# Optimization experiments

Hardware: AMD Instinct MI355X
Metric: run time of the kernel (lower is better)

## Reference

```python
import jax, jax.numpy as jnp
import numpy as np

B, N, K, H = 8, 2048, 30, 128
SCALE = 30.0
EPS = 1e-5


def _gelu(x):
    return jax.nn.gelu(x, approximate=False)


def _lin(x, w, b):
    return x @ w.T + b


def _ln(x, g, b):
    m = x.mean(-1, keepdims=True)
    v = ((x - m) ** 2).mean(-1, keepdims=True)
    return g * (x - m) * jax.lax.rsqrt(v + EPS) + b


def _gather_nodes(h_V, E_idx):
    # h_V: [B,N,H], E_idx: [B,N,K] -> [B,N,K,H]
    b_idx = jnp.arange(h_V.shape[0])[:, None, None]
    return h_V[b_idx, E_idx]


def setup_inputs() -> dict:
    key = jax.random.key(0)
    ks = jax.random.split(key, 16)
    p = 0.02
    inp = {
        'h_V': jax.random.normal(ks[0], (B, N, H), jnp.float32),
        'h_E': jax.random.normal(ks[1], (B, N, K, H), jnp.float32),
        'E_idx': jax.random.randint(ks[2], (B, N, K), 0, N, jnp.int32),
        'mask_V': jnp.ones((B, N), jnp.float32),
        'mask_attend': jnp.ones((B, N, K), jnp.float32),
        # node message MLP (3H -> H -> H -> H)
        'W1_w': jax.random.normal(ks[3], (H, 3 * H), jnp.float32) * p,
        'W1_b': jnp.zeros((H,), jnp.float32),
        'W2_w': jax.random.normal(ks[4], (H, H), jnp.float32) * p,
        'W2_b': jnp.zeros((H,), jnp.float32),
        'W3_w': jax.random.normal(ks[5], (H, H), jnp.float32) * p,
        'W3_b': jnp.zeros((H,), jnp.float32),
        # edge message MLP (3H -> H -> H -> H)
        'W11_w': jax.random.normal(ks[6], (H, 3 * H), jnp.float32) * p,
        'W11_b': jnp.zeros((H,), jnp.float32),
        'W12_w': jax.random.normal(ks[7], (H, H), jnp.float32) * p,
        'W12_b': jnp.zeros((H,), jnp.float32),
        'W13_w': jax.random.normal(ks[8], (H, H), jnp.float32) * p,
        'W13_b': jnp.zeros((H,), jnp.float32),
        # layer norms
        'n1_g': jnp.ones((H,), jnp.float32), 'n1_b': jnp.zeros((H,), jnp.float32),
        'n2_g': jnp.ones((H,), jnp.float32), 'n2_b': jnp.zeros((H,), jnp.float32),
        'n3_g': jnp.ones((H,), jnp.float32), 'n3_b': jnp.zeros((H,), jnp.float32),
        # position-wise FFN (H -> 4H -> H)
        'din_w': jax.random.normal(ks[9], (4 * H, H), jnp.float32) * p,
        'din_b': jnp.zeros((4 * H,), jnp.float32),
        'dout_w': jax.random.normal(ks[10], (H, 4 * H), jnp.float32) * p,
        'dout_b': jnp.zeros((H,), jnp.float32),
    }
    return inp


def reference(h_V, h_E, E_idx, mask_V, mask_attend,
              W1_w, W1_b, W2_w, W2_b, W3_w, W3_b,
              W11_w, W11_b, W12_w, W12_b, W13_w, W13_b,
              n1_g, n1_b, n2_g, n2_b, n3_g, n3_b,
              din_w, din_b, dout_w, dout_b):
    k = h_E.shape[-2]
    # --- node update ---
    h_nbr = _gather_nodes(h_V, E_idx)                       # [B,N,K,H]
    h_V_exp = jnp.broadcast_to(h_V[:, :, None, :], h_nbr.shape)
    h_EV = jnp.concatenate([h_V_exp, h_nbr, h_E], axis=-1)  # [B,N,K,3H]
    h_message = _lin(_gelu(_lin(_gelu(_lin(h_EV, W1_w, W1_b)), W2_w, W2_b)), W3_w, W3_b)
    h_message = mask_attend[..., None] * h_message
    dh = jnp.sum(h_message, axis=-2) / SCALE
    h_V = _ln(h_V + dh, n1_g, n1_b)
    dh = _lin(_gelu(_lin(h_V, din_w, din_b)), dout_w, dout_b)
    h_V = _ln(h_V + dh, n2_g, n2_b)
    h_V = mask_V[..., None] * h_V
    # --- edge update ---
    h_nbr = _gather_nodes(h_V, E_idx)
    h_V_exp = jnp.broadcast_to(h_V[:, :, None, :], h_nbr.shape)
    h_EV = jnp.concatenate([h_V_exp, h_nbr, h_E], axis=-1)
    h_message = _lin(_gelu(_lin(_gelu(_lin(h_EV, W11_w, W11_b)), W12_w, W12_b)), W13_w, W13_b)
    h_E = _ln(h_E + h_message, n3_g, n3_b)
    return (h_V, h_E)
```

## Files before the change

kernel.cpp:

```cpp
#include <hip/hip_runtime.h>

#define B_ 8
#define N_ 2048
#define K_ 30
#define H_ 128
#define LDA 136
#define LDM 132
#define EPS_ 1e-5f

typedef __attribute__((ext_vector_type(8))) short short8;
typedef __attribute__((ext_vector_type(4))) float f32x4;

__device__ inline unsigned short f2bf(float f) {
  union { float f; unsigned u; } v; v.f = f;
  unsigned r = v.u + 0x7fffu + ((v.u >> 16) & 1u);
  return (unsigned short)(r >> 16);
}

__device__ inline float bf2f(unsigned short h) {
  union { unsigned u; float f; } v; v.u = ((unsigned)h) << 16; return v.f;
}

__device__ inline unsigned pkbf(float lo, float hi) {
  unsigned r;
  asm("v_cvt_pk_bf16_f32 %0, %1, %2" : "=v"(r) : "v"(lo), "v"(hi));
  return r;
}

__device__ inline float gelu_t(float x) {
  const float p = x * x;
  const float z = x * (1.5957691216057308f + 0.07135481627f * p);
  const float e = exp2f(z * -1.4426950408889634f);
  return x * __builtin_amdgcn_rcpf(1.0f + e);
}

__device__ inline short8 pack8(float4 a, float4 b) {
  short8 o;
  o[0] = (short)f2bf(a.x); o[1] = (short)f2bf(a.y); o[2] = (short)f2bf(a.z); o[3] = (short)f2bf(a.w);
  o[4] = (short)f2bf(b.x); o[5] = (short)f2bf(b.y); o[6] = (short)f2bf(b.z); o[7] = (short)f2bf(b.w);
  return o;
}

template<int LDW>
__device__ inline void gemmT(const unsigned short* __restrict__ sA,
                             const unsigned short* __restrict__ W,
                             int lane, int cb, f32x4 (&acc)[4][2]) {
  const int rl = lane & 15;
  const int klo = (lane >> 4) << 3;
#pragma unroll
  for (int ks = 0; ks < 4; ++ks) {
    short8 wf[2];
#pragma unroll
    for (int fn = 0; fn < 2; ++fn)
      wf[fn] = *(const short8*)(W + (size_t)(cb + fn * 16 + rl) * LDW + ks * 32 + klo);
#pragma unroll
    for (int et = 0; et < 4; ++et) {
      const short8 ef = *(const short8*)(sA + (et * 16 + rl) * LDA + ks * 32 + klo);
      acc[et][0] = __builtin_amdgcn_mfma_f32_16x16x32_bf16(wf[0], ef, acc[et][0], 0, 0, 0);
      acc[et][1] = __builtin_amdgcn_mfma_f32_16x16x32_bf16(wf[1], ef, acc[et][1], 0, 0, 0);
    }
  }
}

#define ZERO42(A) \
  _Pragma("unroll") for (int e_ = 0; e_ < 4; ++e_) { A[e_][0] = (f32x4){0,0,0,0}; A[e_][1] = (f32x4){0,0,0,0}; }

template<int LDW, int NN>
__device__ inline void gemm64(const unsigned short* __restrict__ sA,
                              const unsigned short* __restrict__ W,
                              int lane, int cb, f32x4 (&acc)[4][NN]) {
  const int rl = lane & 15;
  const int klo = (lane >> 4) << 3;
#pragma unroll
  for (int ks = 0; ks < 4; ++ks) {
    short8 a[4];
#pragma unroll
    for (int m = 0; m < 4; ++m)
      a[m] = *(const short8*)(sA + (m * 16 + rl) * LDA + ks * 32 + klo);
#pragma unroll
    for (int n = 0; n < NN; ++n) {
      const short8 b8 = *(const short8*)(W + (size_t)(cb + n * 16 + rl) * LDW + ks * 32 + klo);
#pragma unroll
      for (int m = 0; m < 4; ++m)
        acc[m][n] = __builtin_amdgcn_mfma_f32_16x16x32_bf16(a[m], b8, acc[m][n], 0, 0, 0);
    }
  }
}

__global__ __launch_bounds__(256) void prep(const float* __restrict__ w1, const float* __restrict__ w2,
                                            const float* __restrict__ w3, const float* __restrict__ w11,
                                            const float* __restrict__ w12, const float* __restrict__ w13,
                                            const float* __restrict__ din, const float* __restrict__ dout,
                                            unsigned short* __restrict__ dst) {
  const int i = blockIdx.x * 256 + threadIdx.x;
  const float* s; int off;
  if (i < 49152)       { s = w1;  off = 0; }
  else if (i < 65536)  { s = w2;  off = 49152; }
  else if (i < 81920)  { s = w3;  off = 65536; }
  else if (i < 131072) { s = w11; off = 81920; }
  else if (i < 147456) { s = w12; off = 131072; }
  else if (i < 163840) { s = w13; off = 147456; }
  else if (i < 229376) { s = din; off = 163840; }
  else                 { s = dout; off = 229376; }
  dst[i] = f2bf(s[i - off]);
}

template<bool F32SRC, bool SPLIT>
__global__ __launch_bounds__(256) void preY(const void* __restrict__ Xv,
                                            const unsigned short* __restrict__ Wbase,
                                            unsigned short* __restrict__ Yc,
                                            unsigned short* __restrict__ Yn) {
  __shared__ __align__(16) unsigned short sA[64 * LDA];
  const int tid = threadIdx.x;
  const int lane = tid & 63;
  const int w = tid >> 6;
  const int rows = blockIdx.x << 6;
  const int rl = lane & 15;
  const int h4 = (lane >> 4) << 2;

  if (F32SRC) {
    const float* X = (const float*)Xv;
    for (int t = tid; t < 1024; t += 256) {
      const int r = t >> 4, seg = t & 15;
      const float* src = X + (((size_t)(rows + r)) << 7) + seg * 8;
      *(short8*)(sA + r * LDA + seg * 8) = pack8(*(const float4*)src, *(const float4*)(src + 4));
    }
  } else {
    const unsigned short* X = (const unsigned short*)Xv;
    for (int t = tid; t < 1024; t += 256) {
      const int r = t >> 4, seg = t & 15;
      *(short8*)(sA + r * LDA + seg * 8) =
          *(const short8*)(X + (((size_t)(rows + r)) << 7) + seg * 8);
    }
  }
  __syncthreads();

  const int half = w >> 1;
  const int cb = (w & 1) * 64;
  f32x4 acc[4][4];
#pragma unroll
  for (int m = 0; m < 4; ++m)
#pragma unroll
    for (int n = 0; n < 4; ++n) acc[m][n] = (f32x4){0, 0, 0, 0};
  gemm64<384, 4>(sA, Wbase + half * 128, lane, cb, acc);

  unsigned short* Y = half ? Yn : Yc;
  const int stride = SPLIT ? 128 : 256;
  const int coff = SPLIT ? 0 : half * 128;
#pragma unroll
  for (int n = 0; n < 4; ++n) {
    const int col = coff + cb + n * 16 + rl;
#pragma unroll
    for (int m = 0; m < 4; ++m)
#pragma unroll
      for (int i = 0; i < 4; ++i)
        Y[(size_t)(rows + m * 16 + h4 + i) * stride + col] = f2bf(acc[m][n][i]);
  }
}

__global__ __launch_bounds__(256, 4) void k1(
    const float* __restrict__ hV, const float* __restrict__ hE,
    const int* __restrict__ Eidx, const float* __restrict__ mattend,
    const unsigned short* __restrict__ wc, const unsigned short* __restrict__ Y1,
    const float* __restrict__ W1b, const float* __restrict__ W2b,
    const float* __restrict__ W3b, const float* __restrict__ n1g,
    const float* __restrict__ n1b, unsigned short* __restrict__ hV1b,
    float* __restrict__ outE) {
  __shared__ __align__(16) unsigned short sBuf[2 * 64 * LDA];
  __shared__ __align__(16) unsigned short sYc[2 * 128];
  __shared__ float sMask[64];
  __shared__ float sRed[2][128];
  unsigned short* sE = sBuf;
  unsigned short* sG = sBuf + 64 * LDA;
  float* sM = (float*)sBuf;

  const int tid = threadIdx.x;
  const int lane = tid & 63;
  const int w = tid >> 6;
  const int rl = lane & 15;
  const int h4 = (lane >> 4) << 2;
  const int bid = (blockIdx.x & 7) * 1024 + (blockIdx.x >> 3);
  const int v0 = bid << 1;
  const int b = v0 >> 11;
  const int n0 = v0 & (N_ - 1);
  const int bBase = b * N_;

  const unsigned short* W1c = wc;
  const unsigned short* W2c = wc + 49152;
  const unsigned short* W3c = wc + 65536;

  for (int t = tid; t < 1024; t += 256) {
    const int r = t >> 4, seg = t & 15;
    const int g = r >> 5, kk = r & 31;
    const int kc = kk < K_ ? kk : K_ - 1;
    const size_t e = (size_t)(bBase + n0 + g) * K_ + kc;
    const float* src = hE + (e << 7) + seg * 8;
    const short8 o = pack8(*(const float4*)src, *(const float4*)(src + 4));
    *(short8*)(sE + r * LDA + seg * 8) = o;
    if (kk < K_)
      *(short8*)((unsigned short*)(outE + (e << 7)) + 128 + seg * 8) = o;
  }
  for (int t = tid; t < 1024; t += 256) {
    const int r = t >> 4, seg = t & 15;
    const int g = r >> 5;
    int kk = r & 31; if (kk >= K_) kk = K_ - 1;
    const int j = Eidx[(bBase + n0 + g) * K_ + kk];
    *(short8*)(sG + r * LDA + seg * 8) =
        *(const short8*)(Y1 + (size_t)(bBase + j) * 256 + 128 + seg * 8);
  }
  {
    const int g = tid >> 7, c = tid & 127;
    sYc[g * 128 + c] = Y1[(size_t)(bBase + n0 + g) * 256 + c];
  }
  if (tid < 64) {
    const int g = tid >> 5, kk = tid & 31;
    sMask[tid] = (kk < K_) ? mattend[(bBase + n0 + g) * K_ + kk] : 0.f;
  }
  __syncthreads();

  f32x4 acc[4][2];
  ZERO42(acc)
  gemmT<384>(sE, W1c + 256, lane, w * 32, acc);

  {
    float4 b1v[2];
    b1v[0] = *(const float4*)(W1b + w * 32 + h4);
    b1v[1] = *(const float4*)(W1b + w * 32 + 16 + h4);
#pragma unroll
    for (int et = 0; et < 4; ++et) {
      const int e = et * 16 + rl;
      const int g = et >> 1;
#pragma unroll
      for (int fn = 0; fn < 2; ++fn) {
        const int f0 = w * 32 + fn * 16 + h4;
        const ushort4 yc = *(const ushort4*)(sYc + g * 128 + f0);
        const ushort4 yn = *(const ushort4*)(sG + e * LDA + f0);
        const float x0 = gelu_t(acc[et][fn][0] + b1v[fn].x + bf2f(yc.x) + bf2f(yn.x));
        const float x1 = gelu_t(acc[et][fn][1] + b1v[fn].y + bf2f(yc.y) + bf2f(yn.y));
        const float x2 = gelu_t(acc[et][fn][2] + b1v[fn].z + bf2f(yc.z) + bf2f(yn.z));
        const float x3 = gelu_t(acc[et][fn][3] + b1v[fn].w + bf2f(yc.w) + bf2f(yn.w));
        uint2 o; o.x = pkbf(x0, x1); o.y = pkbf(x2, x3);
        *(uint2*)(sG + e * LDA + f0) = o;
      }
    }
  }
  __syncthreads();

  f32x4 acc2[4][2];
  ZERO42(acc2)
  gemmT<128>(sG, W2c, lane, w * 32, acc2);
  __syncthreads();
  {
    float4 b2v[2];
    b2v[0] = *(const float4*)(W2b + w * 32 + h4);
    b2v[1] = *(const float4*)(W2b + w * 32 + 16 + h4);
#pragma unroll
    for (int et = 0; et < 4; ++et) {
      const int e = et * 16 + rl;
#pragma unroll
      for (int fn = 0; fn < 2; ++fn) {
        const int f0 = w * 32 + fn * 16 + h4;
        const float x0 = gelu_t(acc2[et][fn][0] + b2v[fn].x);
        const float x1 = gelu_t(acc2[et][fn][1] + b2v[fn].y);
        const float x2 = gelu_t(acc2[et][fn][2] + b2v[fn].z);
        const float x3 = gelu_t(acc2[et][fn][3] + b2v[fn].w);
        uint2 o; o.x = pkbf(x0, x1); o.y = pkbf(x2, x3);
        *(uint2*)(sG + e * LDA + f0) = o;
      }
    }
  }
  __syncthreads();

  f32x4 acc3[4][2];
  ZERO42(acc3)
  gemmT<128>(sG, W3c, lane, w * 32, acc3);
  __syncthreads();

  {
    float4 b3v[2];
    b3v[0] = *(const float4*)(W3b + w * 32 + h4);
    b3v[1] = *(const float4*)(W3b + w * 32 + 16 + h4);
#pragma unroll
    for (int et = 0; et < 4; ++et) {
      const int e = et * 16 + rl;
      const float mk = sMask[e];
#pragma unroll
      for (int fn = 0; fn < 2; ++fn) {
        const int f0 = w * 32 + fn * 16 + h4;
        const float4 v = make_float4((acc3[et][fn][0] + b3v[fn].x) * mk,
                                     (acc3[et][fn][1] + b3v[fn].y) * mk,
                                     (acc3[et][fn][2] + b3v[fn].z) * mk,
                                     (acc3[et][fn][3] + b3v[fn].w) * mk);
        *(float4*)(sM + e * LDM + f0) = v;
      }
    }
  }
  __syncthreads();

  {
    const int g = tid >> 7, f = tid & 127;
    float s = 0.f;
#pragma unroll
    for (int kk = 0; kk < 32; ++kk) s += sM[(g * 32 + kk) * LDM + f];
    sRed[g][f] = s;
  }
  __syncthreads();

  if (w < 2) {
    const size_t base = ((size_t)(bBase + n0 + w)) << 7;
    const float x0 = hV[base + lane] + sRed[w][lane] * (1.0f / 30.0f);
    const float x1 = hV[base + 64 + lane] + sRed[w][64 + lane] * (1.0f / 30.0f);
    float s = x0 + x1;
#pragma unroll
    for (int o = 1; o < 64; o <<= 1) s += __shfl_xor(s, o);
    const float mean = s * (1.0f / 128.0f);
    const float d0 = x0 - mean, d1 = x1 - mean;
    float vs = d0 * d0 + d1 * d1;
#pragma unroll
    for (int o = 1; o < 64; o <<= 1) vs += __shfl_xor(vs, o);
    const float inv = rsqrtf(vs * (1.0f / 128.0f) + EPS_);
    hV1b[base + lane] = f2bf(n1g[lane] * (d0 * inv) + n1b[lane]);
    hV1b[base + 64 + lane] = f2bf(n1g[64 + lane] * (d1 * inv) + n1b[64 + lane]);
  }
}

__global__ __launch_bounds__(256) void k2(
    const unsigned short* __restrict__ hV1b, const unsigned short* __restrict__ wc,
    const float* __restrict__ dinb, const float* __restrict__ doutb,
    const float* __restrict__ n2g, const float* __restrict__ n2b,
    const float* __restrict__ maskV, float* __restrict__ outV,
    unsigned short* __restrict__ hV2c) {
  __shared__ __align__(16) unsigned short sT[16 * LDA];
  __shared__ float sStat[16][2][4];

  const int tid = threadIdx.x;
  const int lane = tid & 63;
  const int w = tid >> 6;
  const int rl = lane & 15;
  const int h4 = (lane >> 4) << 2;
  const int klo = (lane >> 4) << 3;
  const int rowbase = blockIdx.x << 4;

  const unsigned short* dinc = wc + 163840;
  const unsigned short* doutc = wc + 229376;

  short8 ef[4];
#pragma unroll
  for (int ks = 0; ks < 4; ++ks)
    ef[ks] = *(const short8*)(hV1b + (((size_t)(rowbase + rl)) << 7) + ks * 32 + klo);

  f32x4 acc2[2];
  acc2[0] = (f32x4){0, 0, 0, 0}; acc2[1] = (f32x4){0, 0, 0, 0};

  for (int c = 0; c < 4; ++c) {
    f32x4 acc1[2];
    acc1[0] = (f32x4){0, 0, 0, 0}; acc1[1] = (f32x4){0, 0, 0, 0};
#pragma unroll
    for (int ks = 0; ks < 4; ++ks)
#pragma unroll
      for (int fn = 0; fn < 2; ++fn) {
        const short8 wf = *(const short8*)(dinc + (size_t)(c * 128 + w * 32 + fn * 16 + rl) * 128 + ks * 32 + klo);
        acc1[fn] = __builtin_amdgcn_mfma_f32_16x16x32_bf16(wf, ef[ks], acc1[fn], 0, 0, 0);
      }
    __syncthreads();
    {
      float4 db[2];
      db[0] = *(const float4*)(dinb + c * 128 + w * 32 + h4);
      db[1] = *(const float4*)(dinb + c * 128 + w * 32 + 16 + h4);
#pragma unroll
      for (int fn = 0; fn < 2; ++fn) {
        const int f0 = w * 32 + fn * 16 + h4;
        const float x0 = gelu_t(acc1[fn][0] + db[fn].x);
        const float x1 = gelu_t(acc1[fn][1] + db[fn].y);
        const float x2 = gelu_t(acc1[fn][2] + db[fn].z);
        const float x3 = gelu_t(acc1[fn][3] + db[fn].w);
        uint2 o; o.x = pkbf(x0, x1); o.y = pkbf(x2, x3);
        *(uint2*)(sT + rl * LDA + f0) = o;
      }
    }
    __syncthreads();
#pragma unroll
    for (int ks = 0; ks < 4; ++ks) {
      const short8 xf = *(const short8*)(sT + rl * LDA + ks * 32 + klo);
#pragma unroll
      for (int fn = 0; fn < 2; ++fn) {
        const short8 wf2 = *(const short8*)(doutc + (size_t)(w * 32 + fn * 16 + rl) * 512 + c * 128 + ks * 32 + klo);
        acc2[fn] = __builtin_amdgcn_mfma_f32_16x16x32_bf16(wf2, xf, acc2[fn], 0, 0, 0);
      }
    }
  }

  const int row = rl;
  const int grow = rowbase + row;
  {
    float4 wbv[2];
    wbv[0] = *(const float4*)(doutb + w * 32 + h4);
    wbv[1] = *(const float4*)(doutb + w * 32 + 16 + h4);
    float s = 0.f, ss = 0.f;
#pragma unroll
    for (int fn = 0; fn < 2; ++fn) {
      const int f0 = w * 32 + fn * 16 + h4;
      const ushort4 rr = *(const ushort4*)(hV1b + (((size_t)grow) << 7) + f0);
      const float x0 = acc2[fn][0] + wbv[fn].x + bf2f(rr.x);
      const float x1 = acc2[fn][1] + wbv[fn].y + bf2f(rr.y);
      const float x2 = acc2[fn][2] + wbv[fn].z + bf2f(rr.z);
      const float x3 = acc2[fn][3] + wbv[fn].w + bf2f(rr.w);
      acc2[fn] = (f32x4){x0, x1, x2, x3};
      s += x0 + x1 + x2 + x3;
      ss += x0 * x0 + x1 * x1 + x2 * x2 + x3 * x3;
    }
    s += __shfl_xor(s, 16); s += __shfl_xor(s, 32);
    ss += __shfl_xor(ss, 16); ss += __shfl_xor(ss, 32);
    if (lane < 16) { sStat[row][0][w] = s; sStat[row][1][w] = ss; }
  }
  __syncthreads();
  {
    const float sum = sStat[row][0][0] + sStat[row][0][1] + sStat[row][0][2] + sStat[row][0][3];
    const float ssq = sStat[row][1][0] + sStat[row][1][1] + sStat[row][1][2] + sStat[row][1][3];
    const float mean = sum * (1.0f / 128.0f);
    const float inv = rsqrtf(ssq * (1.0f / 128.0f) - mean * mean + EPS_);
    const float mv = maskV[grow];
#pragma unroll
    for (int fn = 0; fn < 2; ++fn) {
      const int f0 = w * 32 + fn * 16 + h4;
      const float4 gv = *(const float4*)(n2g + f0);
      const float4 bv = *(const float4*)(n2b + f0);
      const float y0 = (gv.x * (acc2[fn][0] - mean) * inv + bv.x) * mv;
      const float y1 = (gv.y * (acc2[fn][1] - mean) * inv + bv.y) * mv;
      const float y2 = (gv.z * (acc2[fn][2] - mean) * inv + bv.z) * mv;
      const float y3 = (gv.w * (acc2[fn][3] - mean) * inv + bv.w) * mv;
      *(float4*)(outV + (((size_t)grow) << 7) + f0) = make_float4(y0, y1, y2, y3);
      uint2 o; o.x = pkbf(y0, y1); o.y = pkbf(y2, y3);
      *(uint2*)(hV2c + (((size_t)grow) << 7) + f0) = o;
    }
  }
}

__global__ __launch_bounds__(256, 4) void k3(
    const int* __restrict__ Eidx, const unsigned short* __restrict__ wc,
    const unsigned short* __restrict__ Y2c, const unsigned short* __restrict__ Y2n,
    const float* __restrict__ W11b, const float* __restrict__ W12b,
    const float* __restrict__ W13b, const float* __restrict__ n3g,
    const float* __restrict__ n3b, float* __restrict__ outE) {
  __shared__ __align__(16) unsigned short sE[64 * LDA];
  __shared__ __align__(16) unsigned short sG[64 * LDA];
  __shared__ unsigned short sYc[2 * 128];
  __shared__ float sStat[64][2][4];

  const int tid = threadIdx.x;
  const int lane = tid & 63;
  const int w = tid >> 6;
  const int rl = lane & 15;
  const int h4 = (lane >> 4) << 2;
  const int bid = (blockIdx.x & 7) * 1024 + (blockIdx.x >> 3);
  const int v0 = bid << 1;
  const int b = v0 >> 11;
  const int n0 = v0 & (N_ - 1);
  const int bBase = b * N_;

  const unsigned short* W11c = wc + 81920;
  const unsigned short* W12c = wc + 131072;
  const unsigned short* W13c = wc + 147456;

  for (int t = tid; t < 1024; t += 256) {
    const int r = t >> 4, seg = t & 15;
    const int g = r >> 5;
    int kk = r & 31; if (kk >= K_) kk = K_ - 1;
    const size_t e = (size_t)(bBase + n0 + g) * K_ + kk;
    *(short8*)(sE + r * LDA + seg * 8) =
        *(const short8*)((const unsigned short*)(outE + (e << 7)) + 128 + seg * 8);
  }
  for (int t = tid; t < 1024; t += 256) {
    const int r = t >> 4, seg = t & 15;
    const int g = r >> 5;
    int kk = r & 31; if (kk >= K_) kk = K_ - 1;
    const int j = Eidx[(bBase + n0 + g) * K_ + kk];
    *(short8*)(sG + r * LDA + seg * 8) =
        *(const short8*)(Y2n + (size_t)(bBase + j) * 128 + seg * 8);
  }
  {
    const int g = tid >> 7, c = tid & 127;
    sYc[g * 128 + c] = Y2c[(size_t)(bBase + n0 + g) * 128 + c];
  }
  __syncthreads();

  f32x4 acc[4][2];
  ZERO42(acc)
  gemm64<384, 2>(sE, W11c + 256, lane, w * 32, acc);

#pragma unroll
  for (int n = 0; n < 2; ++n) {
    const int f = w * 32 + n * 16 + rl;
    const float bb = W11b[f];
#pragma unroll
    for (int m = 0; m < 4; ++m)
#pragma unroll
      for (int i = 0; i < 4; ++i) {
        const int e = m * 16 + h4 + i;
        const float x = acc[m][n][i] + bb + bf2f(sYc[(e >> 5) * 128 + f]) + bf2f(sG[e * LDA + f]);
        sG[e * LDA + f] = f2bf(gelu_t(x));
      }
  }
  __syncthreads();

  f32x4 acc2[4][2];
  ZERO42(acc2)
  gemm64<128, 2>(sG, W12c, lane, w * 32, acc2);
  __syncthreads();
#pragma unroll
  for (int n = 0; n < 2; ++n) {
    const int f = w * 32 + n * 16 + rl;
    const float bb = W12b[f];
#pragma unroll
    for (int m = 0; m < 4; ++m)
#pragma unroll
      for (int i = 0; i < 4; ++i) {
        const int e = m * 16 + h4 + i;
        sG[e * LDA + f] = f2bf(gelu_t(acc2[m][n][i] + bb));
      }
  }
  __syncthreads();

  f32x4 acc3[4][2];
  ZERO42(acc3)
  gemm64<128, 2>(sG, W13c, lane, w * 32, acc3);

  float gc[2], bc[2], wb[2];
#pragma unroll
  for (int n = 0; n < 2; ++n) {
    const int f = w * 32 + n * 16 + rl;
    gc[n] = n3g[f]; bc[n] = n3b[f]; wb[n] = W13b[f];
  }
#pragma unroll
  for (int m = 0; m < 4; ++m)
#pragma unroll
    for (int i = 0; i < 4; ++i) {
      const int e = m * 16 + h4 + i;
      float s = 0.f, ss = 0.f;
#pragma unroll
      for (int n = 0; n < 2; ++n) {
        const int f = w * 32 + n * 16 + rl;
        const float x = acc3[m][n][i] + wb[n] + bf2f(sE[e * LDA + f]);
        acc3[m][n][i] = x;
        s += x; ss += x * x;
      }
#pragma unroll
      for (int o = 1; o <= 8; o <<= 1) { s += __shfl_xor(s, o); ss += __shfl_xor(ss, o); }
      if (rl == 0) { sStat[e][0][w] = s; sStat[e][1][w] = ss; }
    }
  __syncthreads();
#pragma unroll
  for (int m = 0; m < 4; ++m)
#pragma unroll
    for (int i = 0; i < 4; ++i) {
      const int e = m * 16 + h4 + i;
      const int g = e >> 5, kk = e & 31;
      if (kk >= K_) continue;
      const float sum = sStat[e][0][0] + sStat[e][0][1] + sStat[e][0][2] + sStat[e][0][3];
      const float ssq = sStat[e][1][0] + sStat[e][1][1] + sStat[e][1][2] + sStat[e][1][3];
      const float mean = sum * (1.0f / 128.0f);
      const float inv = rsqrtf(ssq * (1.0f / 128.0f) - mean * mean + EPS_);
      float* dst = outE + (((size_t)((bBase + n0 + g) * K_ + kk)) << 7) + w * 32 + rl;
#pragma unroll
      for (int n = 0; n < 2; ++n)
        dst[n * 16] = gc[n] * (acc3[m][n][i] - mean) * inv + bc[n];
    }
}

extern "C" void kernel_launch(void* const* d_in, const int* in_sizes, int n_in,
                              void* d_out, int out_size, void* d_ws, size_t ws_size,
                              hipStream_t stream) {
  const float* hV = (const float*)d_in[0];
  const float* hE = (const float*)d_in[1];
  const int* Eidx = (const int*)d_in[2];
  const float* maskV = (const float*)d_in[3];
  const float* mattend = (const float*)d_in[4];
  const float* W1w = (const float*)d_in[5];   const float* W1b = (const float*)d_in[6];
  const float* W2w = (const float*)d_in[7];   const float* W2b = (const float*)d_in[8];
  const float* W3w = (const float*)d_in[9];   const float* W3b = (const float*)d_in[10];
  const float* W11w = (const float*)d_in[11]; const float* W11b = (const float*)d_in[12];
  const float* W12w = (const float*)d_in[13]; const float* W12b = (const float*)d_in[14];
  const float* W13w = (const float*)d_in[15]; const float* W13b = (const float*)d_in[16];
  const float* n1g = (const float*)d_in[17];  const float* n1b = (const float*)d_in[18];
  const float* n2g = (const float*)d_in[19];  const float* n2b = (const float*)d_in[20];
  const float* n3g = (const float*)d_in[21];  const float* n3b = (const float*)d_in[22];
  const float* dinw = (const float*)d_in[23]; const float* dinb = (const float*)d_in[24];
  const float* doutw = (const float*)d_in[25]; const float* doutb = (const float*)d_in[26];

  unsigned short* wc   = (unsigned short*)d_ws;
  unsigned short* R1   = wc + 294912;
  unsigned short* R2   = R1 + 4194304;
  unsigned short* Y1   = R1;
  unsigned short* hV1b = R2;
  unsigned short* hV2c = R1;
  unsigned short* Y2c  = R1 + 2097152;
  unsigned short* Y2n  = R2;

  float* outV = (float*)d_out;
  float* outE = outV + (size_t)B_ * N_ * H_;

  prep<<<1152, 256, 0, stream>>>(W1w, W2w, W3w, W11w, W12w, W13w, dinw, doutw, wc);
  preY<true, false><<<256, 256, 0, stream>>>(hV, wc, Y1, Y1);
  k1<<<8192, 256, 0, stream>>>(hV, hE, Eidx, mattend, wc, Y1,
                               W1b, W2b, W3b, n1g, n1b, hV1b, outE);
  k2<<<1024, 256, 0, stream>>>(hV1b, wc, dinb, doutb, n2g, n2b, maskV, outV, hV2c);
  preY<false, true><<<256, 256, 0, stream>>>(hV2c, wc + 81920, Y2c, Y2n);
  k3<<<8192, 256, 0, stream>>>(Eidx, wc, Y2c, Y2n,
                               W11b, W12b, W13b, n3g, n3b, outE);
}
```

Before: 460.6 us.

## Share one LDS buffer per block, re-read fp32 h_E in k3, raise occupancy

k1 and k3 now use one 64-row LDS tile instead of two. The edge tile is consumed by the first GEMM before the gathered neighbour rows are loaded into the same buffer, and the k1 message reduction stores bf16 instead of fp32. This halves LDS per block, so launch bounds rise to 8 blocks per CU. k1 no longer stashes bf16 h_E into the output buffer; k3 re-reads fp32 h_E from global for its GEMM input and the residual, which adds HBM traffic and an extra barrier in exchange for occupancy. The residual now uses fp32 h_E rather than the bf16 copy. Conversion helpers switch to the packed hardware bf16 convert.

```diff
diff --git a/kernel.cpp b/kernel.cpp
--- a/kernel.cpp
+++ b/kernel.cpp
@@ -5,26 +5,21 @@
 #define K_ 30
 #define H_ 128
 #define LDA 136
-#define LDM 132
 #define EPS_ 1e-5f
 
 typedef __attribute__((ext_vector_type(8))) short short8;
 typedef __attribute__((ext_vector_type(4))) float f32x4;
-
-__device__ inline unsigned short f2bf(float f) {
-  union { float f; unsigned u; } v; v.f = f;
-  unsigned r = v.u + 0x7fffu + ((v.u >> 16) & 1u);
-  return (unsigned short)(r >> 16);
-}
-
-__device__ inline float bf2f(unsigned short h) {
-  union { unsigned u; float f; } v; v.u = ((unsigned)h) << 16; return v.f;
-}
 
 __device__ inline unsigned pkbf(float lo, float hi) {
   unsigned r;
   asm("v_cvt_pk_bf16_f32 %0, %1, %2" : "=v"(r) : "v"(lo), "v"(hi));
   return r;
+}
+
+__device__ inline unsigned short f2bf(float f) { return (unsigned short)pkbf(f, f); }
+
+__device__ inline float bf2f(unsigned short h) {
+  union { unsigned u; float f; } v; v.u = ((unsigned)h) << 16; return v.f;
 }
 
 __device__ inline float gelu_t(float x) {
@@ -35,10 +30,10 @@
 }
 
 __device__ inline short8 pack8(float4 a, float4 b) {
-  short8 o;
-  o[0] = (short)f2bf(a.x); o[1] = (short)f2bf(a.y); o[2] = (short)f2bf(a.z); o[3] = (short)f2bf(a.w);
-  o[4] = (short)f2bf(b.x); o[5] = (short)f2bf(b.y); o[6] = (short)f2bf(b.z); o[7] = (short)f2bf(b.w);
-  return o;
+  union { unsigned u[4]; short8 s; } v;
+  v.u[0] = pkbf(a.x, a.y); v.u[1] = pkbf(a.z, a.w);
+  v.u[2] = pkbf(b.x, b.y); v.u[3] = pkbf(b.z, b.w);
+  return v.s;
 }
 
 template<int LDW>
@@ -158,21 +153,17 @@
   }
 }
 
-__global__ __launch_bounds__(256, 4) void k1(
+__global__ __launch_bounds__(256, 8) void k1(
     const float* __restrict__ hV, const float* __restrict__ hE,
     const int* __restrict__ Eidx, const float* __restrict__ mattend,
     const unsigned short* __restrict__ wc, const unsigned short* __restrict__ Y1,
     const float* __restrict__ W1b, const float* __restrict__ W2b,
     const float* __restrict__ W3b, const float* __restrict__ n1g,
-    const float* __restrict__ n1b, unsigned short* __restrict__ hV1b,
-    float* __restrict__ outE) {
-  __shared__ __align__(16) unsigned short sBuf[2 * 64 * LDA];
+    const float* __restrict__ n1b, unsigned short* __restrict__ hV1b) {
+  __shared__ __align__(16) unsigned short sA[64 * LDA];
   __shared__ __align__(16) unsigned short sYc[2 * 128];
   __shared__ float sMask[64];
   __shared__ float sRed[2][128];
-  unsigned short* sE = sBuf;
-  unsigned short* sG = sBuf + 64 * LDA;
-  float* sM = (float*)sBuf;
 
   const int tid = threadIdx.x;
   const int lane = tid & 63;
@@ -191,36 +182,36 @@
 
   for (int t = tid; t < 1024; t += 256) {
     const int r = t >> 4, seg = t & 15;
-    const int g = r >> 5, kk = r & 31;
-    const int kc = kk < K_ ? kk : K_ - 1;
-    const size_t e = (size_t)(bBase + n0 + g) * K_ + kc;
+    const int g = r >> 5;
+    int kk = r & 31; if (kk >= K_) kk = K_ - 1;
+    const size_t e = (size_t)(bBase + n0 + g) * K_ + kk;
     const float* src = hE + (e << 7) + seg * 8;
-    const short8 o = pack8(*(const float4*)src, *(const float4*)(src + 4));
-    *(short8*)(sE + r * LDA + seg * 8) = o;
-    if (kk < K_)
-      *(short8*)((unsigned short*)(outE + (e << 7)) + 128 + seg * 8) = o;
-  }
+    *(short8*)(sA + r * LDA + seg * 8) = pack8(*(const float4*)src, *(const float4*)(src + 4));
+  }
+  {
+    const int g = tid >> 7, c = tid & 127;
+    sYc[g * 128 + c] = Y1[(size_t)(bBase + n0 + g) * 256 + c];
+  }
+  if (tid < 64) {
+    const int g = tid >> 5, kk = tid & 31;
+    sMask[tid] = (kk < K_) ? mattend[(bBase + n0 + g) * K_ + kk] : 0.f;
+  }
+  __syncthreads();
+
+  f32x4 acc[4][2];
+  ZERO42(acc)
+  gemmT<384>(sA, W1c + 256, lane, w * 32, acc);
+  __syncthreads();
+
   for (int t = tid; t < 1024; t += 256) {
     const int r = t >> 4, seg = t & 15;
     const int g = r >> 5;
     int kk = r & 31; if (kk >= K_) kk = K_ - 1;
     const int j = Eidx[(bBase + n0 + g) * K_ + kk];
-    *(short8*)(sG + r * LDA + seg * 8) =
+    *(short8*)(sA + r * LDA + seg * 8) =
         *(const short8*)(Y1 + (size_t)(bBase + j) * 256 + 128 + seg * 8);
   }
-  {
-    const int g = tid >> 7, c = tid & 127;
-    sYc[g * 128 + c] = Y1[(size_t)(bBase + n0 + g) * 256 + c];
-  }
-  if (tid < 64) {
-    const int g = tid >> 5, kk = tid & 31;
-    sMask[tid] = (kk < K_) ? mattend[(bBase + n0 + g) * K_ + kk] : 0.f;
-  }
-  __syncthreads();
-
-  f32x4 acc[4][2];
-  ZERO42(acc)
-  gemmT<384>(sE, W1c + 256, lane, w * 32, acc);
+  __syncthreads();
 
   {
     float4 b1v[2];
@@ -234,13 +225,13 @@
       for (int fn = 0; fn < 2; ++fn) {
         const int f0 = w * 32 + fn * 16 + h4;
         const ushort4 yc = *(const ushort4*)(sYc + g * 128 + f0);
-        const ushort4 yn = *(const ushort4*)(sG + e * LDA + f0);
+        const ushort4 yn = *(const ushort4*)(sA + e * LDA + f0);
         const float x0 = gelu_t(acc[et][fn][0] + b1v[fn].x + bf2f(yc.x) + bf2f(yn.x));
         const float x1 = gelu_t(acc[et][fn][1] + b1v[fn].y + bf2f(yc.y) + bf2f(yn.y));
         const float x2 = gelu_t(acc[et][fn][2] + b1v[fn].z + bf2f(yc.z) + bf2f(yn.z));
         const float x3 = gelu_t(acc[et][fn][3] + b1v[fn].w + bf2f(yc.w) + bf2f(yn.w));
         uint2 o; o.x = pkbf(x0, x1); o.y = pkbf(x2, x3);
-        *(uint2*)(sG + e * LDA + f0) = o;
+        *(uint2*)(sA + e * LDA + f0) = o;
       }
     }
   }
@@ -248,7 +239,7 @@
 
   f32x4 acc2[4][2];
   ZERO42(acc2)
-  gemmT<128>(sG, W2c, lane, w * 32, acc2);
+  gemmT<128>(sA, W2c, lane, w * 32, acc2);
   __syncthreads();
   {
     float4 b2v[2];
@@ -265,7 +256,7 @@
         const float x2 = gelu_t(acc2[et][fn][2] + b2v[fn].z);
         const float x3 = gelu_t(acc2[et][fn][3] + b2v[fn].w);
         uint2 o; o.x = pkbf(x0, x1); o.y = pkbf(x2, x3);
-        *(uint2*)(sG + e * LDA + f0) = o;
+        *(uint2*)(sA + e * LDA + f0) = o;
       }
     }
   }
@@ -273,7 +264,7 @@
 
   f32x4 acc3[4][2];
   ZERO42(acc3)
-  gemmT<128>(sG, W3c, lane, w * 32, acc3);
+  gemmT<128>(sA, W3c, lane, w * 32, acc3);
   __syncthreads();
 
   {
@@ -287,11 +278,10 @@
 #pragma unroll
       for (int fn = 0; fn < 2; ++fn) {
         const int f0 = w * 32 + fn * 16 + h4;
-        const float4 v = make_float4((acc3[et][fn][0] + b3v[fn].x) * mk,
-                                     (acc3[et][fn][1] + b3v[fn].y) * mk,
-                                     (acc3[et][fn][2] + b3v[fn].z) * mk,
-                                     (acc3[et][fn][3] + b3v[fn].w) * mk);
-        *(float4*)(sM + e * LDM + f0) = v;
+        uint2 o;
+        o.x = pkbf((acc3[et][fn][0] + b3v[fn].x) * mk, (acc3[et][fn][1] + b3v[fn].y) * mk);
+        o.y = pkbf((acc3[et][fn][2] + b3v[fn].z) * mk, (acc3[et][fn][3] + b3v[fn].w) * mk);
+        *(uint2*)(sA + e * LDA + f0) = o;
       }
     }
   }
@@ -301,7 +291,7 @@
     const int g = tid >> 7, f = tid & 127;
     float s = 0.f;
 #pragma unroll
-    for (int kk = 0; kk < 32; ++kk) s += sM[(g * 32 + kk) * LDM + f];
+    for (int kk = 0; kk < 32; ++kk) s += bf2f(sA[(g * 32 + kk) * LDA + f]);
     sRed[g][f] = s;
   }
   __syncthreads();
@@ -436,14 +426,14 @@
   }
 }
 
-__global__ __launch_bounds__(256, 4) void k3(
-    const int* __restrict__ Eidx, const unsigned short* __restrict__ wc,
+__global__ __launch_bounds__(256, 8) void k3(
+    const float* __restrict__ hE, const int* __restrict__ Eidx,
+    const unsigned short* __restrict__ wc,
     const unsigned short* __restrict__ Y2c, const unsigned short* __restrict__ Y2n,
     const float* __restrict__ W11b, const float* __restrict__ W12b,
     const float* __restrict__ W13b, const float* __restrict__ n3g,
     const float* __restrict__ n3b, float* __restrict__ outE) {
-  __shared__ __align__(16) unsigned short sE[64 * LDA];
-  __shared__ __align__(16) unsigned short sG[64 * LDA];
+  __shared__ __align__(16) unsigned short sA[64 * LDA];
   __shared__ unsigned short sYc[2 * 128];
   __shared__ float sStat[64][2][4];
 
@@ -467,26 +457,29 @@
     const int g = r >> 5;
     int kk = r & 31; if (kk >= K_) kk = K_ - 1;
     const size_t e = (size_t)(bBase + n0 + g) * K_ + kk;
-    *(short8*)(sE + r * LDA + seg * 8) =
-        *(const short8*)((const unsigned short*)(outE + (e << 7)) + 128 + seg * 8);
-  }
+    const float* src = hE + (e << 7) + seg * 8;
+    *(short8*)(sA + r * LDA + seg * 8) = pack8(*(const float4*)src, *(const float4*)(src + 4));
+  }
+  {
+    const int g = tid >> 7, c = tid & 127;
+    sYc[g * 128 + c] = Y2c[(size_t)(bBase + n0 + g) * 128 + c];
+  }
+  __syncthreads();
+
+  f32x4 acc[4][2];
+  ZERO42(acc)
+  gemm64<384, 2>(sA, W11c + 256, lane, w * 32, acc);
+  __syncthreads();
+
   for (int t = tid; t < 1024; t += 256) {
     const int r = t >> 4, seg = t & 15;
     const int g = r >> 5;
     int kk = r & 31; if (kk >= K_) kk = K_ - 1;
     const int j = Eidx[(bBase + n0 + g) * K_ + kk];
-    *(short8*)(sG + r * LDA + seg * 8) =
+    *(short8*)(sA + r * LDA + seg * 8) =
         *(const short8*)(Y2n + (size_t)(bBase + j) * 128 + seg * 8);
   }
-  {
-    const int g = tid >> 7, c = tid & 127;
-    sYc[g * 128 + c] = Y2c[(size_t)(bBase + n0 + g) * 128 + c];
-  }
-  __syncthreads();
-
-  f32x4 acc[4][2];
-  ZERO42(acc)
-  gemm64<384, 2>(sE, W11c + 256, lane, w * 32, acc);
+  __syncthreads();
 
 #pragma unroll
   for (int n = 0; n < 2; ++n) {
@@ -497,15 +490,15 @@
 #pragma unroll
       for (int i = 0; i < 4; ++i) {
         const int e = m * 16 + h4 + i;
-        const float x = acc[m][n][i] + bb + bf2f(sYc[(e >> 5) * 128 + f]) + bf2f(sG[e * LDA + f]);
-        sG[e * LDA + f] = f2bf(gelu_t(x));
+        const float x = acc[m][n][i] + bb + bf2f(sYc[(e >> 5) * 128 + f]) + bf2f(sA[e * LDA + f]);
+        sA[e * LDA + f] = f2bf(gelu_t(x));
       }
   }
   __syncthreads();
 
   f32x4 acc2[4][2];
   ZERO42(acc2)
-  gemm64<128, 2>(sG, W12c, lane, w * 32, acc2);
+  gemm64<128, 2>(sA, W12c, lane, w * 32, acc2);
   __syncthreads();
 #pragma unroll
   for (int n = 0; n < 2; ++n) {
@@ -516,14 +509,14 @@
 #pragma unroll
       for (int i = 0; i < 4; ++i) {
         const int e = m * 16 + h4 + i;
-        sG[e * LDA + f] = f2bf(gelu_t(acc2[m][n][i] + bb));
+        sA[e * LDA + f] = f2bf(gelu_t(acc2[m][n][i] + bb));
       }
   }
   __syncthreads();
 
   f32x4 acc3[4][2];
   ZERO42(acc3)
-  gemm64<128, 2>(sG, W13c, lane, w * 32, acc3);
+  gemm64<128, 2>(sA, W13c, lane, w * 32, acc3);
 
   float gc[2], bc[2], wb[2];
 #pragma unroll
@@ -536,11 +529,14 @@
 #pragma unroll
     for (int i = 0; i < 4; ++i) {
       const int e = m * 16 + h4 + i;
+      const int g = e >> 5, kk = e & 31;
+      const bool valid = kk < K_;
+      const float* er = hE + (((size_t)((bBase + n0 + g) * K_ + (valid ? kk : K_ - 1))) << 7) + w * 32 + rl;
       float s = 0.f, ss = 0.f;
 #pragma unroll
       for (int n = 0; n < 2; ++n) {
-        const int f = w * 32 + n * 16 + rl;
-        const float x = acc3[m][n][i] + wb[n] + bf2f(sE[e * LDA + f]);
+        float x = acc3[m][n][i] + wb[n];
+        if (valid) x += er[n * 16];
         acc3[m][n][i] = x;
         s += x; ss += x * x;
       }
@@ -602,9 +598,9 @@
   prep<<<1152, 256, 0, stream>>>(W1w, W2w, W3w, W11w, W12w, W13w, dinw, doutw, wc);
   preY<true, false><<<256, 256, 0, stream>>>(hV, wc, Y1, Y1);
   k1<<<8192, 256, 0, stream>>>(hV, hE, Eidx, mattend, wc, Y1,
-                               W1b, W2b, W3b, n1g, n1b, hV1b, outE);
+                               W1b, W2b, W3b, n1g, n1b, hV1b);
   k2<<<1024, 256, 0, stream>>>(hV1b, wc, dinb, doutb, n2g, n2b, maskV, outV, hV2c);
   preY<false, true><<<256, 256, 0, stream>>>(hV2c, wc + 81920, Y2c, Y2n);
-  k3<<<8192, 256, 0, stream>>>(Eidx, wc, Y2c, Y2n,
+  k3<<<8192, 256, 0, stream>>>(hE, Eidx, wc, Y2c, Y2n,
                                W11b, W12b, W13b, n3g, n3b, outE);
 }
```

Result: slower. 697.1 us (+51.4%).
